# Kernel tuning notes

Hardware: AMD Instinct MI355X
Metric: run time of the kernel (lower is better)

## Reference

```python
import jax, jax.numpy as jnp
import numpy as np

MODEL_DIM = 1024
NUM_HEADS = 16
HEAD_DIM = MODEL_DIM // NUM_HEADS
ROPE_BASE = 10000.0


def apply_rope(x):
    # x: [B, H, S, D] -- rotate-half RoPE convention
    S, D = x.shape[-2], x.shape[-1]
    inv_freq = 1.0 / (ROPE_BASE ** (jnp.arange(0, D, 2, dtype=jnp.float32) / D))  # [D/2]
    t = jnp.arange(S, dtype=jnp.float32)
    freqs = t[:, None] * inv_freq[None, :]                  # [S, D/2]
    cos = jnp.concatenate([jnp.cos(freqs), jnp.cos(freqs)], axis=-1)  # [S, D]
    sin = jnp.concatenate([jnp.sin(freqs), jnp.sin(freqs)], axis=-1)
    x1, x2 = x[..., : D // 2], x[..., D // 2 :]
    rot = jnp.concatenate([-x2, x1], axis=-1)
    return x * cos + rot * sin


def setup_inputs() -> dict:
    key = jax.random.key(0)
    k1, k2, k3 = jax.random.split(key, 3)
    B, S, Dm = 4, 2048, MODEL_DIM
    std = 1.0 / np.sqrt(Dm)
    x = jax.random.normal(k1, (B, S, Dm), dtype=jnp.float32)
    w_qkv = jax.random.normal(k2, (Dm, 3 * Dm), dtype=jnp.float32) * std
    b_qkv = jnp.zeros((3 * Dm,), dtype=jnp.float32)
    w_out = jax.random.normal(k3, (Dm, Dm), dtype=jnp.float32) * std
    b_out = jnp.zeros((Dm,), dtype=jnp.float32)
    return {"x": x, "w_qkv": w_qkv, "b_qkv": b_qkv, "w_out": w_out, "b_out": b_out}


def reference(x, w_qkv, b_qkv, w_out, b_out):
    B, S, Dm = x.shape
    H, Dh = NUM_HEADS, HEAD_DIM
    scale = Dh ** -0.5
    qkv = x @ w_qkv + b_qkv                                  # [B, S, 3*Dm]
    qkv = qkv.reshape(B, S, 3, H, Dh).transpose(2, 0, 3, 1, 4)  # [3, B, H, S, Dh]
    q, k, v = qkv[0], qkv[1], qkv[2]
    q = apply_rope(q)
    k = apply_rope(k)
    scores = jnp.einsum("bhqd,bhkd->bhqk", q, k) * scale      # [B, H, S, S]
    causal = jnp.tril(jnp.ones((S, S), dtype=bool))
    scores = jnp.where(causal[None, None], scores, -jnp.inf)
    attn = jax.nn.softmax(scores, axis=-1)
    out = jnp.einsum("bhqk,bhkd->bhqd", attn, v)              # [B, H, S, Dh]
    out = out.transpose(0, 2, 1, 3).reshape(B, S, Dm)
    out = out @ w_out + b_out
    return out, attn
```

## Files before the change

kernel.cpp:

```cpp
#include <hip/hip_runtime.h>
#include <hip/hip_bf16.h>
#include <stdint.h>

typedef unsigned short u16;
typedef __attribute__((ext_vector_type(4))) float f32x4;
typedef __attribute__((ext_vector_type(8))) short s16x8;

#define SEQ 2048
#define NB 4
#define DM 1024
#define NHD 16
#define DH 64

__device__ __forceinline__ u16 f2bf(float f) {
  union { float f; uint32_t u; } v; v.f = f;
  return (u16)((v.u + 0x7FFFu + ((v.u >> 16) & 1u)) >> 16);
}
__device__ __forceinline__ float bf2f(u16 u) {
  union { uint32_t u; float f; } v; v.u = ((uint32_t)u) << 16;
  return v.f;
}
__device__ __forceinline__ void gload16(const u16* g, u16* l) {
  __builtin_amdgcn_global_load_lds((const __attribute__((address_space(1))) void*)g,
                                   (__attribute__((address_space(3))) void*)l, 16, 0, 0);
}

__device__ __forceinline__ void stage64x64_swz(const u16* gbase, long gstride,
                                               u16* lds, int tid) {
  int l = tid & 63, w = tid >> 6;
  int rsub = l >> 3;
  int srcElem = ((l & 7) ^ rsub) * 8;
  #pragma unroll
  for (int p = 0; p < 2; ++p) {
    int row0 = w * 16 + p * 8;
    gload16(gbase + (long)(row0 + rsub) * gstride + srcElem, lds + row0 * 64);
  }
}
__device__ __forceinline__ void stage64x64_swz8(const u16* gbase, long gstride,
                                                u16* lds, int tid) {
  int l = tid & 63, w = tid >> 6;
  int rsub = l >> 3;
  int srcElem = ((l & 7) ^ rsub) * 8;
  int row0 = w * 8;
  gload16(gbase + (long)(row0 + rsub) * gstride + srcElem, lds + row0 * 64);
}
__device__ __forceinline__ s16x8 frag_swz(const u16* lds, int row, int cb) {
  return *(const s16x8*)&lds[row * 64 + (cb ^ ((row & 7) << 3))];
}

__global__ __launch_bounds__(256) void k_cvt(const float* __restrict__ in,
                                             u16* __restrict__ out, int n4) {
  int idx = blockIdx.x * 256 + threadIdx.x;
  int stride = gridDim.x * 256;
  for (; idx < n4; idx += stride) {
    float4 v = ((const float4*)in)[idx];
    ushort4 o;
    o.x = f2bf(v.x); o.y = f2bf(v.y); o.z = f2bf(v.z); o.w = f2bf(v.w);
    ((ushort4*)out)[idx] = o;
  }
}

__global__ __launch_bounds__(256) void k_trig(float2* __restrict__ cs) {
  int t = blockIdx.x * 256 + threadIdx.x;
  int s = t >> 5, ih = t & 31;
  float fq = exp2f(-(float)ih * 0.4152410118609203f);
  float ang = (float)s * fq;
  cs[t] = make_float2(cosf(ang), sinf(ang));
}

__global__ __launch_bounds__(256) void k_tpose(const float* __restrict__ in,
                                               u16* __restrict__ out, int R, int C) {
  __shared__ u16 tile[64][65];
  int c0 = blockIdx.x * 64, r0 = blockIdx.y * 64;
  int tx = threadIdx.x & 63, ty = threadIdx.x >> 6;
  #pragma unroll
  for (int rr = ty; rr < 64; rr += 4)
    tile[rr][tx] = f2bf(in[(long)(r0 + rr) * C + c0 + tx]);
  __syncthreads();
  #pragma unroll
  for (int cc = ty; cc < 64; cc += 4)
    out[(long)(c0 + cc) * R + r0 + tx] = tile[tx][cc];
}

__global__ __launch_bounds__(256) void k_gemm_qkv(const u16* __restrict__ A,
                                                  const u16* __restrict__ Bt,
                                                  const float* __restrict__ bias,
                                                  const float2* __restrict__ cs,
                                                  u16* __restrict__ Qr,
                                                  u16* __restrict__ Kr,
                                                  u16* __restrict__ VtG) {
  const int K = DM;
  __shared__ u16 As[128 * 64];
  __shared__ u16 Bs[128 * 64];
  int tid = threadIdx.x, lane = tid & 63, wave = tid >> 6;
  int wm = (wave >> 1) * 64, wn = (wave & 1) * 64;
  long m0 = (long)blockIdx.y * 128, n0 = (long)blockIdx.x * 128;
  int lrow = lane & 15, lk8 = (lane >> 4) * 8;
  int srow = wave * 8 + (lane >> 3);
  int scol = (lane & 7) * 8;
  const u16* Ag = &A[(m0 + srow) * (long)K + scol];
  const u16* Bg = &Bt[(n0 + srow) * (long)K + scol];
  f32x4 acc[4][4] = {};
  for (int k0 = 0; k0 < K; k0 += 64) {
    __syncthreads();
    #pragma unroll
    for (int p = 0; p < 4; ++p) {
      gload16(Ag + (long)p * 32 * K + k0, &As[(p * 32 + wave * 8) * 64]);
      gload16(Bg + (long)p * 32 * K + k0, &Bs[(p * 32 + wave * 8) * 64]);
    }
    __syncthreads();
    #pragma unroll
    for (int h = 0; h < 2; ++h) {
      s16x8 af[4], bfr[4];
      #pragma unroll
      for (int t = 0; t < 4; ++t)
        af[t]  = *(const s16x8*)&As[(wm + t * 16 + lrow) * 64 + h * 32 + lk8];
      #pragma unroll
      for (int t = 0; t < 4; ++t)
        bfr[t] = *(const s16x8*)&Bs[(wn + t * 16 + lrow) * 64 + h * 32 + lk8];
      #pragma unroll
      for (int i = 0; i < 4; ++i)
        #pragma unroll
        for (int j = 0; j < 4; ++j)
          acc[i][j] = __builtin_amdgcn_mfma_f32_16x16x32_bf16(af[i], bfr[j], acc[i][j], 0, 0, 0);
    }
  }
  int coln = (int)(n0) + wn;
  int sec = coln >> 10;
  int hh = (coln & 1023) >> 6;
  int crow = (lane >> 4) * 4, ccol = lane & 15;
  int rowb = (int)m0 + wm;
  if (sec < 2) {
    u16* dst = (sec == 0) ? Qr : Kr;
    float sc = (sec == 0) ? 0.125f : 1.0f;
    #pragma unroll
    for (int j2 = 0; j2 < 2; ++j2) {
      int ih = j2 * 16 + ccol;
      float bv1 = bias[coln + j2 * 16 + ccol];
      float bv2 = bias[coln + j2 * 16 + ccol + 32];
      #pragma unroll
      for (int i = 0; i < 4; ++i) {
        #pragma unroll
        for (int r = 0; r < 4; ++r) {
          int row = rowb + i * 16 + crow + r;
          int b = row >> 11, s = row & 2047;
          float2 cv = cs[(s << 5) + ih];
          float v1 = acc[i][j2][r] + bv1;
          float v2 = acc[i][j2 + 2][r] + bv2;
          long ob = ((long)((b * NHD + hh) * SEQ + s)) * 64;
          dst[ob + ih]      = f2bf((v1 * cv.x - v2 * cv.y) * sc);
          dst[ob + ih + 32] = f2bf((v2 * cv.x + v1 * cv.y) * sc);
        }
      }
    }
  } else {
    #pragma unroll
    for (int i = 0; i < 4; ++i) {
      int row = rowb + i * 16 + crow;
      int b = row >> 11, sl = row & 2047;
      int jt = sl >> 6, sr = sl & 63;
      #pragma unroll
      for (int j = 0; j < 4; ++j) {
        int d = j * 16 + ccol;
        float bv = bias[coln + j * 16 + ccol];
        long idx = (((long)(b * NHD + hh) * 32 + jt) * 64 + d) * 64 + sr;
        ushort4 o;
        o.x = f2bf(acc[i][j][0] + bv); o.y = f2bf(acc[i][j][1] + bv);
        o.z = f2bf(acc[i][j][2] + bv); o.w = f2bf(acc[i][j][3] + bv);
        *(ushort4*)&VtG[idx] = o;
      }
    }
  }
}

template<int OUT_BF16>
__global__ __launch_bounds__(256) void k_gemm(const u16* __restrict__ A,
                                              const u16* __restrict__ Bt_g,
                                              const float* __restrict__ bias,
                                              void* __restrict__ Cout,
                                              int M, int N, int K) {
  __shared__ u16 As[128 * 64];
  __shared__ u16 Bs[128 * 64];
  int tid = threadIdx.x, lane = tid & 63, wave = tid >> 6;
  int wm = (wave >> 1) * 64, wn = (wave & 1) * 64;
  long m0 = (long)blockIdx.y * 128, n0 = (long)blockIdx.x * 128;
  int lrow = lane & 15, lk8 = (lane >> 4) * 8;
  int srow = wave * 8 + (lane >> 3);
  int scol = (lane & 7) * 8;
  const u16* Ag = &A[(m0 + srow) * (long)K + scol];
  const u16* Bg = &Bt_g[(n0 + srow) * (long)K + scol];
  f32x4 acc[4][4] = {};
  for (int k0 = 0; k0 < K; k0 += 64) {
    __syncthreads();
    #pragma unroll
    for (int p = 0; p < 4; ++p) {
      gload16(Ag + (long)p * 32 * K + k0, &As[(p * 32 + wave * 8) * 64]);
      gload16(Bg + (long)p * 32 * K + k0, &Bs[(p * 32 + wave * 8) * 64]);
    }
    __syncthreads();
    #pragma unroll
    for (int h = 0; h < 2; ++h) {
      s16x8 af[4], bfr[4];
      #pragma unroll
      for (int t = 0; t < 4; ++t)
        af[t]  = *(const s16x8*)&As[(wm + t * 16 + lrow) * 64 + h * 32 + lk8];
      #pragma unroll
      for (int t = 0; t < 4; ++t)
        bfr[t] = *(const s16x8*)&Bs[(wn + t * 16 + lrow) * 64 + h * 32 + lk8];
      #pragma unroll
      for (int i = 0; i < 4; ++i)
        #pragma unroll
        for (int j = 0; j < 4; ++j)
          acc[i][j] = __builtin_amdgcn_mfma_f32_16x16x32_bf16(af[i], bfr[j], acc[i][j], 0, 0, 0);
    }
  }
  int crow = (lane >> 4) * 4, ccol = lane & 15;
  #pragma unroll
  for (int i = 0; i < 4; ++i)
  #pragma unroll
  for (int j = 0; j < 4; ++j) {
    long col = n0 + wn + j * 16 + ccol;
    float bv = bias ? bias[col] : 0.f;
    #pragma unroll
    for (int r = 0; r < 4; ++r) {
      long row = m0 + wm + i * 16 + crow + r;
      float v = acc[i][j][r] + bv;
      if (OUT_BF16) ((u16*)Cout)[row * N + col] = f2bf(v);
      else          ((float*)Cout)[row * N + col] = v;
    }
  }
}

__global__ __launch_bounds__(512) void k_attn(const u16* __restrict__ Qr,
                                              const u16* __restrict__ Kr,
                                              const u16* __restrict__ VtG,
                                              float* __restrict__ attn,
                                              u16* __restrict__ ctx) {
  constexpr int LP = 72;
  __shared__ u16 Ks[64 * 64];
  __shared__ u16 Vs[64 * 64];
  __shared__ u16 Ps[8][16 * LP];
  int tid = threadIdx.x, lane = tid & 63, wave = tid >> 6;
  int wgid = blockIdx.x;
  int c = wgid & 7, t7 = wgid >> 3;
  int bh = c * 8 + (t7 >> 4);
  int qb = 15 - (t7 & 15);
  int q0 = qb * 128;
  int qw0 = q0 + wave * 16;
  int lrow = lane & 15, lg = lane >> 4, lk8 = (lane >> 4) * 8;
  const u16* Qb = Qr + (long)bh * SEQ * 64;
  const u16* Kb = Kr + (long)bh * SEQ * 64;
  const u16* Vtb = VtG + (long)bh * 32 * 4096;
  float* attn_bh = attn + (long)bh * SEQ * SEQ;

  s16x8 qf0 = *(const s16x8*)&Qb[(long)(qw0 + lrow) * 64 + lk8];
  s16x8 qf1 = *(const s16x8*)&Qb[(long)(qw0 + lrow) * 64 + 32 + lk8];

  int njt = 2 * qb + 2;

  float suml[4] = {0.f, 0.f, 0.f, 0.f};
  stage64x64_swz8(Kb, 64, Ks, tid);
  __syncthreads();
  for (int jt = 0; jt < njt; ++jt) {
    const u16* cur = (jt & 1) ? Vs : Ks;
    u16* nxt = (jt & 1) ? Ks : Vs;
    if (jt + 1 < njt)
      stage64x64_swz8(Kb + (long)(jt + 1) * 64 * 64, 64, nxt, tid);
    int dt2 = jt - 2 * qb;
    int wq = (dt2 < 0) ? 100 : (wave - 4 * dt2);
    int ctmax = (wq < 3) ? wq : 3;
    long k0 = (long)jt * 64;
    for (int ct = 0; ct <= ctmax; ++ct) {
      int row = ct * 16 + lrow;
      s16x8 kf0 = frag_swz(cur, row, lk8);
      s16x8 kf1 = frag_swz(cur, row, 32 + lk8);
      f32x4 sa = {0.f, 0.f, 0.f, 0.f};
      sa = __builtin_amdgcn_mfma_f32_16x16x32_bf16(qf0, kf0, sa, 0, 0, 0);
      sa = __builtin_amdgcn_mfma_f32_16x16x32_bf16(qf1, kf1, sa, 0, 0, 0);
      bool diag = (ct == wq);
      int gcol = (int)k0 + ct * 16 + lrow;
      #pragma unroll
      for (int r = 0; r < 4; ++r) {
        int grow = qw0 + lg * 4 + r;
        float e = (!diag || gcol <= grow) ? __expf(sa[r]) : 0.f;
        suml[r] += e;
      }
    }
    __syncthreads();
  }
  #pragma unroll
  for (int r = 0; r < 4; ++r) {
    float v = suml[r];
    v += __shfl_xor(v, 1, 16);
    v += __shfl_xor(v, 2, 16);
    v += __shfl_xor(v, 4, 16);
    v += __shfl_xor(v, 8, 16);
    suml[r] = 1.0f / v;
  }

  f32x4 oacc[4] = {};
  u16* ps = &Ps[wave][0];
  for (int jt = 0; jt < njt; ++jt) {
    __syncthreads();
    stage64x64_swz8(Kb + (long)jt * 64 * 64, 64, Ks, tid);
    stage64x64_swz8(Vtb + jt * 4096, 64, Vs, tid);
    __syncthreads();
    int dt2 = jt - 2 * qb;
    int wq = (dt2 < 0) ? 100 : (wave - 4 * dt2);
    int ctmax = (wq < 3) ? wq : 3;
    long k0 = (long)jt * 64;
    #pragma unroll
    for (int ct = 0; ct < 4; ++ct) {
      if (ct <= ctmax) {
        int row = ct * 16 + lrow;
        s16x8 kf0 = frag_swz(Ks, row, lk8);
        s16x8 kf1 = frag_swz(Ks, row, 32 + lk8);
        f32x4 sa = {0.f, 0.f, 0.f, 0.f};
        sa = __builtin_amdgcn_mfma_f32_16x16x32_bf16(qf0, kf0, sa, 0, 0, 0);
        sa = __builtin_amdgcn_mfma_f32_16x16x32_bf16(qf1, kf1, sa, 0, 0, 0);
        bool diag = (ct == wq);
        int gcol = (int)k0 + ct * 16 + lrow;
        #pragma unroll
        for (int r = 0; r < 4; ++r) {
          int grow = qw0 + lg * 4 + r;
          float e = (!diag || gcol <= grow) ? __expf(sa[r]) : 0.f;
          ps[(lg * 4 + r) * LP + ct * 16 + lrow] = f2bf(e * suml[r]);
        }
      } else {
        #pragma unroll
        for (int r = 0; r < 4; ++r)
          ps[(lg * 4 + r) * LP + ct * 16 + lrow] = 0;
      }
    }
    s16x8 pf0 = *(const s16x8*)&ps[lrow * LP + lk8];
    s16x8 pf1 = *(const s16x8*)&ps[lrow * LP + 32 + lk8];
    #pragma unroll
    for (int dt = 0; dt < 4; ++dt) {
      int row = dt * 16 + lrow;
      s16x8 vf0 = frag_swz(Vs, row, lk8);
      s16x8 vf1 = frag_swz(Vs, row, 32 + lk8);
      oacc[dt] = __builtin_amdgcn_mfma_f32_16x16x32_bf16(pf0, vf0, oacc[dt], 0, 0, 0);
      oacc[dt] = __builtin_amdgcn_mfma_f32_16x16x32_bf16(pf1, vf1, oacc[dt], 0, 0, 0);
    }
    #pragma unroll
    for (int it = 0; it < 4; ++it) {
      int prow = it * 4 + (lane >> 4);
      int c4 = lane & 15;
      ushort4 pv = *(const ushort4*)&ps[prow * LP + c4 * 4];
      f32x4 o;
      o.x = bf2f(pv.x); o.y = bf2f(pv.y); o.z = bf2f(pv.z); o.w = bf2f(pv.w);
      __builtin_nontemporal_store(o,
          (f32x4*)&attn_bh[(long)(qw0 + prow) * SEQ + k0 + c4 * 4]);
    }
  }

  {
    int cstart = q0 + 128;
    int zc4 = (SEQ - cstart) >> 2;
    f32x4 z = {0.f, 0.f, 0.f, 0.f};
    for (int row = 0; row < 128; ++row) {
      f32x4* dst = (f32x4*)&attn_bh[(long)(q0 + row) * SEQ + cstart];
      for (int cc = tid; cc < zc4; cc += 512)
        __builtin_nontemporal_store(z, &dst[cc]);
    }
  }

  int b = bh >> 4, h = bh & 15;
  #pragma unroll
  for (int dt = 0; dt < 4; ++dt)
  #pragma unroll
  for (int r = 0; r < 4; ++r) {
    long grow = qw0 + lg * 4 + r;
    long col = h * 64 + dt * 16 + lrow;
    ctx[((long)b * SEQ + grow) * DM + col] = f2bf(oacc[dt][r]);
  }
}

extern "C" void kernel_launch(void* const* d_in, const int* in_sizes, int n_in,
                              void* d_out, int out_size, void* d_ws, size_t ws_size,
                              hipStream_t stream) {
  const float* x     = (const float*)d_in[0];
  const float* w_qkv = (const float*)d_in[1];
  const float* b_qkv = (const float*)d_in[2];
  const float* w_out = (const float*)d_in[3];
  const float* b_out = (const float*)d_in[4];
  float* outp = (float*)d_out;
  float* attn = outp + (long)NB * SEQ * DM;

  char* ws = (char*)d_ws;
  u16* Qr  = (u16*)(ws);
  u16* Kr  = (u16*)(ws + 16777216L);
  u16* VtG = (u16*)(ws + 33554432L);
  u16* ctx = (u16*)(ws + 50331648L);
  u16* WoT = (u16*)(ws + 67108864L);

  u16*    Xb  = (u16*)attn;
  u16*    WqT = (u16*)((char*)attn + 16777216L);
  float2* cst = (float2*)((char*)attn + 23068672L);

  k_cvt<<<1024, 256, 0, stream>>>(x, Xb, (NB * SEQ * DM) / 4);
  k_trig<<<256, 256, 0, stream>>>(cst);
  k_tpose<<<dim3(3 * DM / 64, DM / 64), 256, 0, stream>>>(w_qkv, WqT, DM, 3 * DM);
  k_tpose<<<dim3(DM / 64, DM / 64), 256, 0, stream>>>(w_out, WoT, DM, DM);

  k_gemm_qkv<<<dim3(3 * DM / 128, NB * SEQ / 128), 256, 0, stream>>>(
      Xb, WqT, b_qkv, cst, Qr, Kr, VtG);

  k_attn<<<1024, 512, 0, stream>>>(Qr, Kr, VtG, attn, ctx);

  k_gemm<0><<<dim3(DM / 128, NB * SEQ / 128), 256, 0, stream>>>(
      ctx, WoT, b_out, outp, NB * SEQ, DM, DM);
}
```

Before: 376.6 us.

## Double-buffer LDS tiles in QKV and output GEMMs with K-step of 32

Both GEMM kernels now use two LDS buffers holding 32-wide K slices. The next slice is prefetched with global_load_lds while MFMAs run on the current one, so each iteration needs one barrier instead of two. The aim is to hide global load latency behind compute. In exchange there are twice as many loop iterations, each doing less work per barrier, and the 64-byte row stride in LDS may cause bank conflicts. Correctness depends on the async LDS load being complete at the single barrier.

```diff
diff --git a/kernel.cpp b/kernel.cpp
--- a/kernel.cpp
+++ b/kernel.cpp
@@ -25,17 +25,6 @@
                                    (__attribute__((address_space(3))) void*)l, 16, 0, 0);
 }
 
-__device__ __forceinline__ void stage64x64_swz(const u16* gbase, long gstride,
-                                               u16* lds, int tid) {
-  int l = tid & 63, w = tid >> 6;
-  int rsub = l >> 3;
-  int srcElem = ((l & 7) ^ rsub) * 8;
-  #pragma unroll
-  for (int p = 0; p < 2; ++p) {
-    int row0 = w * 16 + p * 8;
-    gload16(gbase + (long)(row0 + rsub) * gstride + srcElem, lds + row0 * 64);
-  }
-}
 __device__ __forceinline__ void stage64x64_swz8(const u16* gbase, long gstride,
                                                 u16* lds, int tid) {
   int l = tid & 63, w = tid >> 6;
@@ -82,6 +71,7 @@
     out[(long)(c0 + cc) * R + r0 + tx] = tile[tx][cc];
 }
 
+
 __global__ __launch_bounds__(256) void k_gemm_qkv(const u16* __restrict__ A,
                                                   const u16* __restrict__ Bt,
                                                   const float* __restrict__ bias,
@@ -90,40 +80,43 @@
                                                   u16* __restrict__ Kr,
                                                   u16* __restrict__ VtG) {
   const int K = DM;
-  __shared__ u16 As[128 * 64];
-  __shared__ u16 Bs[128 * 64];
+  __shared__ u16 As[2][128 * 32];
+  __shared__ u16 Bs[2][128 * 32];
   int tid = threadIdx.x, lane = tid & 63, wave = tid >> 6;
   int wm = (wave >> 1) * 64, wn = (wave & 1) * 64;
   long m0 = (long)blockIdx.y * 128, n0 = (long)blockIdx.x * 128;
   int lrow = lane & 15, lk8 = (lane >> 4) * 8;
-  int srow = wave * 8 + (lane >> 3);
-  int scol = (lane & 7) * 8;
+  int srow = wave * 16 + (lane >> 2);
+  int scol = (lane & 3) * 8;
   const u16* Ag = &A[(m0 + srow) * (long)K + scol];
   const u16* Bg = &Bt[(n0 + srow) * (long)K + scol];
   f32x4 acc[4][4] = {};
-  for (int k0 = 0; k0 < K; k0 += 64) {
+  gload16(Ag, &As[0][(wave * 16) * 32]);
+  gload16(Ag + 64L * K, &As[0][(64 + wave * 16) * 32]);
+  gload16(Bg, &Bs[0][(wave * 16) * 32]);
+  gload16(Bg + 64L * K, &Bs[0][(64 + wave * 16) * 32]);
+  __syncthreads();
+  int cur = 0;
+  for (int t = 0; t < K / 32; ++t) {
+    if (t + 1 < K / 32) {
+      int k1 = (t + 1) * 32;
+      gload16(Ag + k1, &As[cur ^ 1][(wave * 16) * 32]);
+      gload16(Ag + 64L * K + k1, &As[cur ^ 1][(64 + wave * 16) * 32]);
+      gload16(Bg + k1, &Bs[cur ^ 1][(wave * 16) * 32]);
+      gload16(Bg + 64L * K + k1, &Bs[cur ^ 1][(64 + wave * 16) * 32]);
+    }
+    s16x8 af[4], bfr[4];
+    #pragma unroll
+    for (int q = 0; q < 4; ++q) af[q]  = *(const s16x8*)&As[cur][(wm + q * 16 + lrow) * 32 + lk8];
+    #pragma unroll
+    for (int q = 0; q < 4; ++q) bfr[q] = *(const s16x8*)&Bs[cur][(wn + q * 16 + lrow) * 32 + lk8];
+    #pragma unroll
+    for (int i = 0; i < 4; ++i)
+      #pragma unroll
+      for (int j = 0; j < 4; ++j)
+        acc[i][j] = __builtin_amdgcn_mfma_f32_16x16x32_bf16(af[i], bfr[j], acc[i][j], 0, 0, 0);
     __syncthreads();
-    #pragma unroll
-    for (int p = 0; p < 4; ++p) {
-      gload16(Ag + (long)p * 32 * K + k0, &As[(p * 32 + wave * 8) * 64]);
-      gload16(Bg + (long)p * 32 * K + k0, &Bs[(p * 32 + wave * 8) * 64]);
-    }
-    __syncthreads();
-    #pragma unroll
-    for (int h = 0; h < 2; ++h) {
-      s16x8 af[4], bfr[4];
-      #pragma unroll
-      for (int t = 0; t < 4; ++t)
-        af[t]  = *(const s16x8*)&As[(wm + t * 16 + lrow) * 64 + h * 32 + lk8];
-      #pragma unroll
-      for (int t = 0; t < 4; ++t)
-        bfr[t] = *(const s16x8*)&Bs[(wn + t * 16 + lrow) * 64 + h * 32 + lk8];
-      #pragma unroll
-      for (int i = 0; i < 4; ++i)
-        #pragma unroll
-        for (int j = 0; j < 4; ++j)
-          acc[i][j] = __builtin_amdgcn_mfma_f32_16x16x32_bf16(af[i], bfr[j], acc[i][j], 0, 0, 0);
-    }
+    cur ^= 1;
   }
   int coln = (int)(n0) + wn;
   int sec = coln >> 10;
@@ -179,40 +172,43 @@
                                               const float* __restrict__ bias,
                                               void* __restrict__ Cout,
                                               int M, int N, int K) {
-  __shared__ u16 As[128 * 64];
-  __shared__ u16 Bs[128 * 64];
+  __shared__ u16 As[2][128 * 32];
+  __shared__ u16 Bs[2][128 * 32];
   int tid = threadIdx.x, lane = tid & 63, wave = tid >> 6;
   int wm = (wave >> 1) * 64, wn = (wave & 1) * 64;
   long m0 = (long)blockIdx.y * 128, n0 = (long)blockIdx.x * 128;
   int lrow = lane & 15, lk8 = (lane >> 4) * 8;
-  int srow = wave * 8 + (lane >> 3);
-  int scol = (lane & 7) * 8;
+  int srow = wave * 16 + (lane >> 2);
+  int scol = (lane & 3) * 8;
   const u16* Ag = &A[(m0 + srow) * (long)K + scol];
   const u16* Bg = &Bt_g[(n0 + srow) * (long)K + scol];
   f32x4 acc[4][4] = {};
-  for (int k0 = 0; k0 < K; k0 += 64) {
+  gload16(Ag, &As[0][(wave * 16) * 32]);
+  gload16(Ag + 64L * K, &As[0][(64 + wave * 16) * 32]);
+  gload16(Bg, &Bs[0][(wave * 16) * 32]);
+  gload16(Bg + 64L * K, &Bs[0][(64 + wave * 16) * 32]);
+  __syncthreads();
+  int cur = 0;
+  for (int t = 0; t < K / 32; ++t) {
+    if (t + 1 < K / 32) {
+      int k1 = (t + 1) * 32;
+      gload16(Ag + k1, &As[cur ^ 1][(wave * 16) * 32]);
+      gload16(Ag + 64L * K + k1, &As[cur ^ 1][(64 + wave * 16) * 32]);
+      gload16(Bg + k1, &Bs[cur ^ 1][(wave * 16) * 32]);
+      gload16(Bg + 64L * K + k1, &Bs[cur ^ 1][(64 + wave * 16) * 32]);
+    }
+    s16x8 af[4], bfr[4];
+    #pragma unroll
+    for (int q = 0; q < 4; ++q) af[q]  = *(const s16x8*)&As[cur][(wm + q * 16 + lrow) * 32 + lk8];
+    #pragma unroll
+    for (int q = 0; q < 4; ++q) bfr[q] = *(const s16x8*)&Bs[cur][(wn + q * 16 + lrow) * 32 + lk8];
+    #pragma unroll
+    for (int i = 0; i < 4; ++i)
+      #pragma unroll
+      for (int j = 0; j < 4; ++j)
+        acc[i][j] = __builtin_amdgcn_mfma_f32_16x16x32_bf16(af[i], bfr[j], acc[i][j], 0, 0, 0);
     __syncthreads();
-    #pragma unroll
-    for (int p = 0; p < 4; ++p) {
-      gload16(Ag + (long)p * 32 * K + k0, &As[(p * 32 + wave * 8) * 64]);
-      gload16(Bg + (long)p * 32 * K + k0, &Bs[(p * 32 + wave * 8) * 64]);
-    }
-    __syncthreads();
-    #pragma unroll
-    for (int h = 0; h < 2; ++h) {
-      s16x8 af[4], bfr[4];
-      #pragma unroll
-      for (int t = 0; t < 4; ++t)
-        af[t]  = *(const s16x8*)&As[(wm + t * 16 + lrow) * 64 + h * 32 + lk8];
-      #pragma unroll
-      for (int t = 0; t < 4; ++t)
-        bfr[t] = *(const s16x8*)&Bs[(wn + t * 16 + lrow) * 64 + h * 32 + lk8];
-      #pragma unroll
-      for (int i = 0; i < 4; ++i)
-        #pragma unroll
-        for (int j = 0; j < 4; ++j)
-          acc[i][j] = __builtin_amdgcn_mfma_f32_16x16x32_bf16(af[i], bfr[j], acc[i][j], 0, 0, 0);
-    }
+    cur ^= 1;
   }
   int crow = (lane >> 4) * 4, ccol = lane & 15;
   #pragma unroll
```

After: 383.3 us. About the same (+1.8%).

## Pipeline QKV GEMM with double-buffered async LDS loads and 128x256 tiles

Applied to the files above, without the earlier changes.

Rewrites the QKV projection GEMM to use 512-thread blocks computing 128x256 tiles. K-slices of 32 are split into halves and double-buffered in LDS, with explicit vmcnt waits so global-to-LDS loads overlap the MFMA work. It also adds an XOR swizzle on the LDS layout to avoid bank conflicts, remaps block IDs for L2 locality, and raises MFMA priority with setprio. In exchange it uses more LDS and relies on hand-counted waitcnt values being correct.

```diff
diff --git a/kernel.cpp b/kernel.cpp
--- a/kernel.cpp
+++ b/kernel.cpp
@@ -25,17 +25,6 @@
                                    (__attribute__((address_space(3))) void*)l, 16, 0, 0);
 }
 
-__device__ __forceinline__ void stage64x64_swz(const u16* gbase, long gstride,
-                                               u16* lds, int tid) {
-  int l = tid & 63, w = tid >> 6;
-  int rsub = l >> 3;
-  int srcElem = ((l & 7) ^ rsub) * 8;
-  #pragma unroll
-  for (int p = 0; p < 2; ++p) {
-    int row0 = w * 16 + p * 8;
-    gload16(gbase + (long)(row0 + rsub) * gstride + srcElem, lds + row0 * 64);
-  }
-}
 __device__ __forceinline__ void stage64x64_swz8(const u16* gbase, long gstride,
                                                 u16* lds, int tid) {
   int l = tid & 63, w = tid >> 6;
@@ -46,6 +35,25 @@
 }
 __device__ __forceinline__ s16x8 frag_swz(const u16* lds, int row, int cb) {
   return *(const s16x8*)&lds[row * 64 + (cb ^ ((row & 7) << 3))];
+}
+
+__device__ __forceinline__ void stageA128(const u16* Ag, int kcol, u16* dst, int tid) {
+  int l = tid & 63, w = tid >> 6;
+  int row = w * 16 + (l >> 2);
+  int gs = (l & 3) ^ ((row >> 1) & 3);
+  gload16(Ag + (long)row * 1024 + kcol + gs * 8, dst + (w * 16) * 32);
+}
+__device__ __forceinline__ void stageB256(const u16* Bg, int kcol, u16* dst, int tid) {
+  int l = tid & 63, w = tid >> 6;
+  #pragma unroll
+  for (int p = 0; p < 2; ++p) {
+    int row = w * 32 + p * 16 + (l >> 2);
+    int gs = (l & 3) ^ ((row >> 1) & 3);
+    gload16(Bg + (long)row * 1024 + kcol + gs * 8, dst + (w * 32 + p * 16) * 32);
+  }
+}
+__device__ __forceinline__ s16x8 fragk32(const u16* slice, int row, int cg) {
+  return *(const s16x8*)&slice[row * 32 + (cg ^ ((row >> 1) & 3)) * 8];
 }
 
 __global__ __launch_bounds__(256) void k_cvt(const float* __restrict__ in,
@@ -82,50 +90,71 @@
     out[(long)(c0 + cc) * R + r0 + tx] = tile[tx][cc];
 }
 
-__global__ __launch_bounds__(256) void k_gemm_qkv(const u16* __restrict__ A,
-                                                  const u16* __restrict__ Bt,
-                                                  const float* __restrict__ bias,
-                                                  const float2* __restrict__ cs,
-                                                  u16* __restrict__ Qr,
-                                                  u16* __restrict__ Kr,
-                                                  u16* __restrict__ VtG) {
-  const int K = DM;
-  __shared__ u16 As[128 * 64];
-  __shared__ u16 Bs[128 * 64];
+__global__ __launch_bounds__(512, 2) void k_gemm_qkv(const u16* __restrict__ A,
+                                                     const u16* __restrict__ Bt,
+                                                     const float* __restrict__ bias,
+                                                     const float2* __restrict__ cs,
+                                                     u16* __restrict__ Qr,
+                                                     u16* __restrict__ Kr,
+                                                     u16* __restrict__ VtG) {
+  __shared__ __align__(16) u16 As[2][2][128 * 32];
+  __shared__ __align__(16) u16 Bs[2][2][256 * 32];
   int tid = threadIdx.x, lane = tid & 63, wave = tid >> 6;
-  int wm = (wave >> 1) * 64, wn = (wave & 1) * 64;
-  long m0 = (long)blockIdx.y * 128, n0 = (long)blockIdx.x * 128;
-  int lrow = lane & 15, lk8 = (lane >> 4) * 8;
-  int srow = wave * 8 + (lane >> 3);
-  int scol = (lane & 7) * 8;
-  const u16* Ag = &A[(m0 + srow) * (long)K + scol];
-  const u16* Bg = &Bt[(n0 + srow) * (long)K + scol];
+  int id = ((int)blockIdx.x & 7) * 96 + ((int)blockIdx.x >> 3);
+  int bx = id % 12, by = id / 12;
+  long m0 = (long)by * 128, n0 = (long)bx * 256;
+  int wm = (wave >> 2) * 64, wn = (wave & 3) * 64;
+  int lrow = lane & 15, cg = lane >> 4;
+  const u16* Ag = A + m0 * 1024;
+  const u16* Bg = Bt + n0 * 1024;
   f32x4 acc[4][4] = {};
-  for (int k0 = 0; k0 < K; k0 += 64) {
-    __syncthreads();
-    #pragma unroll
-    for (int p = 0; p < 4; ++p) {
-      gload16(Ag + (long)p * 32 * K + k0, &As[(p * 32 + wave * 8) * 64]);
-      gload16(Bg + (long)p * 32 * K + k0, &Bs[(p * 32 + wave * 8) * 64]);
-    }
-    __syncthreads();
-    #pragma unroll
-    for (int h = 0; h < 2; ++h) {
-      s16x8 af[4], bfr[4];
-      #pragma unroll
-      for (int t = 0; t < 4; ++t)
-        af[t]  = *(const s16x8*)&As[(wm + t * 16 + lrow) * 64 + h * 32 + lk8];
-      #pragma unroll
-      for (int t = 0; t < 4; ++t)
-        bfr[t] = *(const s16x8*)&Bs[(wn + t * 16 + lrow) * 64 + h * 32 + lk8];
-      #pragma unroll
-      for (int i = 0; i < 4; ++i)
-        #pragma unroll
-        for (int j = 0; j < 4; ++j)
-          acc[i][j] = __builtin_amdgcn_mfma_f32_16x16x32_bf16(af[i], bfr[j], acc[i][j], 0, 0, 0);
-    }
-  }
-  int coln = (int)(n0) + wn;
+
+  auto compute = [&](const u16* aS, const u16* bS) {
+    s16x8 af[4], bf[4];
+    #pragma unroll
+    for (int i = 0; i < 4; ++i) af[i] = fragk32(aS, wm + i * 16 + lrow, cg);
+    #pragma unroll
+    for (int j = 0; j < 4; ++j) bf[j] = fragk32(bS, wn + j * 16 + lrow, cg);
+    __builtin_amdgcn_s_setprio(1);
+    #pragma unroll
+    for (int i = 0; i < 4; ++i)
+      #pragma unroll
+      for (int j = 0; j < 4; ++j)
+        acc[i][j] = __builtin_amdgcn_mfma_f32_16x16x32_bf16(af[i], bf[j], acc[i][j], 0, 0, 0);
+    __builtin_amdgcn_s_setprio(0);
+  };
+
+  stageA128(Ag, 0,  &As[0][0][0], tid); stageB256(Bg, 0,  &Bs[0][0][0], tid);
+  stageA128(Ag, 32, &As[0][1][0], tid); stageB256(Bg, 32, &Bs[0][1][0], tid);
+  stageA128(Ag, 64, &As[1][0][0], tid); stageB256(Bg, 64, &Bs[1][0][0], tid);
+
+  for (int t = 0; t < 15; ++t) {
+    int buf = t & 1;
+    asm volatile("s_waitcnt vmcnt(6)" ::: "memory");
+    __builtin_amdgcn_s_barrier();
+    asm volatile("" ::: "memory");
+    stageA128(Ag, (t + 1) * 64 + 32, &As[buf ^ 1][1][0], tid);
+    stageB256(Bg, (t + 1) * 64 + 32, &Bs[buf ^ 1][1][0], tid);
+    compute(&As[buf][0][0], &Bs[buf][0][0]);
+    asm volatile("s_waitcnt vmcnt(6)" ::: "memory");
+    __builtin_amdgcn_s_barrier();
+    asm volatile("" ::: "memory");
+    if (t + 2 < 16) {
+      stageA128(Ag, (t + 2) * 64, &As[buf][0][0], tid);
+      stageB256(Bg, (t + 2) * 64, &Bs[buf][0][0], tid);
+    }
+    compute(&As[buf][1][0], &Bs[buf][1][0]);
+  }
+  asm volatile("s_waitcnt vmcnt(3)" ::: "memory");
+  __builtin_amdgcn_s_barrier();
+  asm volatile("" ::: "memory");
+  compute(&As[1][0][0], &Bs[1][0][0]);
+  asm volatile("s_waitcnt vmcnt(0)" ::: "memory");
+  __builtin_amdgcn_s_barrier();
+  asm volatile("" ::: "memory");
+  compute(&As[1][1][0], &Bs[1][1][0]);
+
+  int coln = (int)n0 + wn;
   int sec = coln >> 10;
   int hh = (coln & 1023) >> 6;
   int crow = (lane >> 4) * 4, ccol = lane & 15;
@@ -403,8 +432,7 @@
   k_tpose<<<dim3(3 * DM / 64, DM / 64), 256, 0, stream>>>(w_qkv, WqT, DM, 3 * DM);
   k_tpose<<<dim3(DM / 64, DM / 64), 256, 0, stream>>>(w_out, WoT, DM, DM);
 
-  k_gemm_qkv<<<dim3(3 * DM / 128, NB * SEQ / 128), 256, 0, stream>>>(
-      Xb, WqT, b_qkv, cst, Qr, Kr, VtG);
+  k_gemm_qkv<<<768, 512, 0, stream>>>(Xb, WqT, b_qkv, cst, Qr, Kr, VtG);
 
   k_attn<<<1024, 512, 0, stream>>>(Qr, Kr, VtG, attn, ctx);
 
```

Result: slower. 386.1 us (+2.5%).
